# Kernel optimization log

Measured on AMD Instinct MI355X. Metric: run time of the kernel, lower is better.

Reference implementation:

```python
import jax, jax.numpy as jnp
import numpy as np

B, C, M, K, V, D, H, A, L, HF = 2, 128, 4, 4, 64, 1024, 16, 64, 4, 2048
E = M + K
EPS = 1e-5
THETA = 10000.0


def _rmsnorm(x, w):
    return x * jax.lax.rsqrt(jnp.mean(x * x, -1, keepdims=True) + EPS) * w


def _l2norm(x):
    n = jnp.sqrt(jnp.sum(x * x, -1, keepdims=True))
    return x / jnp.maximum(n, EPS)


def _rope(x, cos, sin):
    x1, x2 = jnp.split(x, 2, axis=-1)
    return jnp.concatenate([x1 * cos + x2 * sin, -x1 * sin + x2 * cos], -1)


def _forward(x_input, dec_w1, dec_w2, pos_emb, Wqkv, Wo, Wup, Wdown, attn_norm_w, ffn_norm_w, doc):
    b = x_input.shape[0]
    c = x_input.shape[1] // M
    # decoder_w1 then 'b (c m) (k v) -> b c k (m v)', decoder_w2, pos emb
    x = jnp.einsum('bsd,od->bso', x_input, dec_w1)
    x = x.reshape(b, c, M, K, V).transpose(0, 1, 3, 2, 4).reshape(b, c, K, M * V)
    x = jnp.einsum('bcku,du->bckd', x, dec_w2) + pos_emb
    # decoder_include_original_token: prepend original m tokens per block
    x = jnp.concatenate([x_input.reshape(b, c, M, D), x], axis=2).reshape(b, c * E, D)
    s = c * E
    # mask_mod (decoder_global_original_attn): (causal & kv%e<k & same_doc) | same_block
    idx = jnp.arange(s)
    blk = idx // E
    docs = doc[:, blk]  # [b, s]
    doc_m = docs[:, :, None] == docs[:, None, :]
    causal = blk[:, None] >= blk[None, :]
    kv_ok = (idx % E) < K
    same = blk[:, None] == blk[None, :]
    mask = (causal[None] & kv_ok[None, None, :] & doc_m) | same[None]  # [b, s, s]
    # rotary tables (applied post head-split, dim A)
    inv_freq = (1.0 / THETA) ** (jnp.arange(0, A, 2) / A)
    freqs = jnp.arange(s)[:, None] * inv_freq[None, :]
    cos, sin = jnp.cos(freqs), jnp.sin(freqs)  # [s, A/2]
    scale = 1.0 / jnp.sqrt(jnp.float32(A))
    neg = jnp.float32(-1e30)

    def heads(t):
        return t.reshape(b, s, H, A).transpose(0, 2, 1, 3)

    for li in range(L):
        xn = _rmsnorm(x, attn_norm_w[li])
        qkv = jnp.einsum('bsd,od->bso', xn, Wqkv[li])
        q, k, v = jnp.split(qkv, 3, axis=-1)
        q, k, v = heads(q), heads(k), heads(v)
        q, k = _l2norm(q), _l2norm(k)  # qk_norm
        q, k = _rope(q, cos, sin), _rope(k, cos, sin)
        scores = jnp.einsum('bhqa,bhka->bhqk', q, k) * scale
        scores = jnp.where(mask[:, None], scores, neg)
        probs = jax.nn.softmax(scores, axis=-1)
        attn = jnp.einsum('bhqk,bhka->bhqa', probs, v)
        attn = attn.transpose(0, 2, 1, 3).reshape(b, s, D)
        x1_in = jnp.einsum('bsd,od->bso', attn, Wo[li]) + x
        xf = _rmsnorm(x1_in, ffn_norm_w[li])
        up = jnp.einsum('bsd,od->bso', xf, Wup[li])
        u1, u2 = jnp.split(up, 2, axis=-1)
        x = jnp.einsum('bsh,dh->bsd', jax.nn.silu(u1) * u2, Wdown[li]) + x1_in
    # 'b (c e) d -> (b c) e d' then drop original tokens
    return x.reshape(b * c, E, D)[:, M:]


def setup_inputs() -> dict:
    key = jax.random.key(0)
    ks = jax.random.split(key, 10)
    sc = 0.02
    return {
        'x_input': jax.random.normal(ks[0], (B, C * M, D), jnp.float32),
        'doc': jnp.sort(jax.random.randint(ks[1], (B, C), 0, 4), axis=-1),
        'dec_w1': jax.random.normal(ks[2], (K * V, D), jnp.float32) * sc,
        'dec_w2': jax.random.normal(ks[3], (D, M * V), jnp.float32) * sc,
        'pos_emb': jax.random.normal(ks[4], (1, 1, K, D), jnp.float32) * sc,
        'Wqkv': jax.random.normal(ks[5], (L, 3 * D, D), jnp.float32) * sc,
        'Wo': jax.random.normal(ks[6], (L, D, D), jnp.float32) * sc,
        'Wup': jax.random.normal(ks[7], (L, 2 * HF, D), jnp.float32) * sc,
        'Wdown': jax.random.normal(ks[8], (L, D, HF), jnp.float32) * sc,
        'attn_norm_w': jnp.ones((L, D), jnp.float32),
        'ffn_norm_w': jnp.ones((L, D), jnp.float32),
    }


def reference(x_input, doc, dec_w1, dec_w2, pos_emb, Wqkv, Wo, Wup, Wdown, attn_norm_w, ffn_norm_w):
    return _forward(x_input, dec_w1, dec_w2, pos_emb, Wqkv, Wo, Wup, Wdown, attn_norm_w, ffn_norm_w, doc)
```

## Files before the change

### kernel.cpp

```cpp
#include <hip/hip_runtime.h>
#include <hip/hip_bf16.h>

typedef __bf16 bf16;
typedef __bf16 bf16x8 __attribute__((ext_vector_type(8)));
typedef __bf16 bf16x4 __attribute__((ext_vector_type(4)));
typedef float  f32x4  __attribute__((ext_vector_type(4)));

#define MFMA16(a, b, c) __builtin_amdgcn_mfma_f32_16x16x32_bf16(a, b, c, 0, 0, 0)

template <int EPI, int AF32, int BF32, int TM, int TN>
__global__ __launch_bounds__(256) void gemm_bt(
    const void* __restrict__ Av, const void* __restrict__ Bv,
    const float* __restrict__ Res, void* __restrict__ Out,
    int Ntot, int Ktot, int lda)
{
    constexpr int PA = TM / 64, PB = TN / 64;
    constexpr int WN = (TN == 128) ? ((TM == 128) ? 2 : 4) : 2;
    constexpr int WM = 4 / WN;
    constexpr int I = TM / (WM * 16), J = TN / (WN * 16);
    __shared__ __align__(16) bf16 As[2][TM][40];
    __shared__ __align__(16) bf16 Bs[2][TN][40];
    const int tid  = threadIdx.x;
    const int wave = tid >> 6, lane = tid & 63;
    const int quad = lane >> 4, l16 = lane & 15;
    const int wm = wave / WN, wn = wave % WN;
    const int rowW = wm * (TM / WM), colW = wn * (TN / WN);
    const int rowBase = blockIdx.y * TM, colBase = blockIdx.x * TN;

    f32x4 acc[I][J];
    const f32x4 z4 = {0.f, 0.f, 0.f, 0.f};
#pragma unroll
    for (int i = 0; i < I; i++)
#pragma unroll
        for (int j = 0; j < J; j++) acc[i][j] = z4;

    float4 rAf[PA][2]; bf16x8 rAb[PA];
    float4 rBf[PB][2]; bf16x8 rBb[PB];

    auto loadTile = [&](int kt) {
#pragma unroll
        for (int p = 0; p < PA; p++) {
            int ch = p * 256 + tid, r = ch >> 2, c8 = (ch & 3) << 3;
            if (AF32) {
                const float* s = (const float*)Av + (size_t)(rowBase + r) * lda + kt + c8;
                rAf[p][0] = *(const float4*)s; rAf[p][1] = *(const float4*)(s + 4);
            } else {
                rAb[p] = *(const bf16x8*)((const bf16*)Av + (size_t)(rowBase + r) * lda + kt + c8);
            }
        }
#pragma unroll
        for (int p = 0; p < PB; p++) {
            int ch = p * 256 + tid, r = ch >> 2, c8 = (ch & 3) << 3;
            if (BF32) {
                const float* s = (const float*)Bv + (size_t)(colBase + r) * Ktot + kt + c8;
                rBf[p][0] = *(const float4*)s; rBf[p][1] = *(const float4*)(s + 4);
            } else {
                rBb[p] = *(const bf16x8*)((const bf16*)Bv + (size_t)(colBase + r) * Ktot + kt + c8);
            }
        }
    };
    auto storeTile = [&](int buf) {
#pragma unroll
        for (int p = 0; p < PA; p++) {
            int ch = p * 256 + tid, r = ch >> 2, c8 = (ch & 3) << 3;
            bf16x8 t;
            if (AF32) {
                t[0]=(bf16)rAf[p][0].x; t[1]=(bf16)rAf[p][0].y; t[2]=(bf16)rAf[p][0].z; t[3]=(bf16)rAf[p][0].w;
                t[4]=(bf16)rAf[p][1].x; t[5]=(bf16)rAf[p][1].y; t[6]=(bf16)rAf[p][1].z; t[7]=(bf16)rAf[p][1].w;
            } else t = rAb[p];
            *(bf16x8*)&As[buf][r][c8] = t;
        }
#pragma unroll
        for (int p = 0; p < PB; p++) {
            int ch = p * 256 + tid, r = ch >> 2, c8 = (ch & 3) << 3;
            bf16x8 t;
            if (BF32) {
                t[0]=(bf16)rBf[p][0].x; t[1]=(bf16)rBf[p][0].y; t[2]=(bf16)rBf[p][0].z; t[3]=(bf16)rBf[p][0].w;
                t[4]=(bf16)rBf[p][1].x; t[5]=(bf16)rBf[p][1].y; t[6]=(bf16)rBf[p][1].z; t[7]=(bf16)rBf[p][1].w;
            } else t = rBb[p];
            *(bf16x8*)&Bs[buf][r][c8] = t;
        }
    };

    loadTile(0);
    storeTile(0);
    __syncthreads();
    const int nk = Ktot >> 5;
    for (int k = 0; k < nk; k++) {
        const bool more = (k + 1) < nk;
        if (more) loadTile((k + 1) << 5);
        const int buf = k & 1;
        bf16x8 af[I], bfr[J];
#pragma unroll
        for (int i = 0; i < I; i++)
            af[i] = *(const bf16x8*)&As[buf][rowW + i * 16 + l16][quad * 8];
#pragma unroll
        for (int j = 0; j < J; j++)
            bfr[j] = *(const bf16x8*)&Bs[buf][colW + j * 16 + l16][quad * 8];
#pragma unroll
        for (int i = 0; i < I; i++)
#pragma unroll
            for (int j = 0; j < J; j++)
                acc[i][j] = MFMA16(af[i], bfr[j], acc[i][j]);
        if (more) { storeTile(buf ^ 1); __syncthreads(); }
    }

#pragma unroll
    for (int i = 0; i < I; i++) {
        int row0 = rowBase + rowW + i * 16 + quad * 4;
#pragma unroll
        for (int j = 0; j < J; j++) {
            int col = colBase + colW + j * 16 + l16;
#pragma unroll
            for (int r = 0; r < 4; r++) {
                size_t off = (size_t)(row0 + r) * Ntot + col;
                float v = acc[i][j][r];
                if (EPI == 0)      ((bf16*)Out)[off]  = (bf16)v;
                else if (EPI == 1) ((float*)Out)[off] = v + Res[off];
                else               ((float*)Out)[off] = v;
            }
        }
    }
}

__global__ __launch_bounds__(256) void gemm_up_swiglu(
    const bf16* __restrict__ A, const float* __restrict__ B,
    bf16* __restrict__ Out)
{
    __shared__ __align__(16) bf16 As[2][128][40];
    __shared__ __align__(16) bf16 Bs[2][128][40];
    const int tid  = threadIdx.x;
    const int wave = tid >> 6, lane = tid & 63;
    const int quad = lane >> 4, l16 = lane & 15;
    const int wm = wave >> 1, wn = wave & 1;
    const int rowBase = blockIdx.y * 128, cb = blockIdx.x;

    f32x4 acc[4][4];
    const f32x4 z4 = {0.f, 0.f, 0.f, 0.f};
#pragma unroll
    for (int i = 0; i < 4; i++)
#pragma unroll
        for (int j = 0; j < 4; j++) acc[i][j] = z4;

    bf16x8 rA[2]; float4 rB[2][2];
    auto loadTile = [&](int kt) {
#pragma unroll
        for (int p = 0; p < 2; p++) {
            int ch = p * 256 + tid, r = ch >> 2, c8 = (ch & 3) << 3;
            rA[p] = *(const bf16x8*)(A + (size_t)(rowBase + r) * 1024 + kt + c8);
            int brow = (r >> 6) * 2048 + cb * 64 + (r & 63);
            const float* s = B + (size_t)brow * 1024 + kt + c8;
            rB[p][0] = *(const float4*)s; rB[p][1] = *(const float4*)(s + 4);
        }
    };
    auto storeTile = [&](int buf) {
#pragma unroll
        for (int p = 0; p < 2; p++) {
            int ch = p * 256 + tid, r = ch >> 2, c8 = (ch & 3) << 3;
            *(bf16x8*)&As[buf][r][c8] = rA[p];
            bf16x8 t;
            t[0]=(bf16)rB[p][0].x; t[1]=(bf16)rB[p][0].y; t[2]=(bf16)rB[p][0].z; t[3]=(bf16)rB[p][0].w;
            t[4]=(bf16)rB[p][1].x; t[5]=(bf16)rB[p][1].y; t[6]=(bf16)rB[p][1].z; t[7]=(bf16)rB[p][1].w;
            *(bf16x8*)&Bs[buf][r][c8] = t;
        }
    };

    loadTile(0);
    storeTile(0);
    __syncthreads();
    for (int k = 0; k < 32; k++) {
        const bool more = k < 31;
        if (more) loadTile((k + 1) << 5);
        const int buf = k & 1;
        bf16x8 af[4], bfr[4];
#pragma unroll
        for (int i = 0; i < 4; i++)
            af[i] = *(const bf16x8*)&As[buf][wm * 64 + i * 16 + l16][quad * 8];
#pragma unroll
        for (int j = 0; j < 4; j++) {
            int brow = (j < 2) ? (wn * 32 + j * 16) : (64 + wn * 32 + (j - 2) * 16);
            bfr[j] = *(const bf16x8*)&Bs[buf][brow + l16][quad * 8];
        }
#pragma unroll
        for (int i = 0; i < 4; i++)
#pragma unroll
            for (int j = 0; j < 4; j++)
                acc[i][j] = MFMA16(af[i], bfr[j], acc[i][j]);
        if (more) { storeTile(buf ^ 1); __syncthreads(); }
    }

#pragma unroll
    for (int i = 0; i < 4; i++) {
        int row0 = rowBase + wm * 64 + i * 16 + quad * 4;
#pragma unroll
        for (int jj = 0; jj < 2; jj++) {
            int col = cb * 64 + wn * 32 + jj * 16 + l16;
#pragma unroll
            for (int r = 0; r < 4; r++) {
                float u1 = acc[i][jj][r], u2 = acc[i][jj + 2][r];
                float g = u1 / (1.f + __expf(-u1));
                Out[(size_t)(row0 + r) * 2048 + col] = (bf16)(g * u2);
            }
        }
    }
}

__global__ __launch_bounds__(256) void rmsnorm_k(
    const float* __restrict__ X, const float* __restrict__ W,
    bf16* __restrict__ Out)
{
    const int row = blockIdx.x, tid = threadIdx.x;
    const float4 xv = *(const float4*)(X + (size_t)row * 1024 + tid * 4);
    float ss = xv.x * xv.x + xv.y * xv.y + xv.z * xv.z + xv.w * xv.w;
#pragma unroll
    for (int m = 1; m < 64; m <<= 1) ss += __shfl_xor(ss, m);
    __shared__ float red[4];
    if ((tid & 63) == 0) red[tid >> 6] = ss;
    __syncthreads();
    float tot = red[0] + red[1] + red[2] + red[3];
    float sc = rsqrtf(tot * (1.0f / 1024.0f) + 1e-5f);
    const float4 wv = *(const float4*)(W + tid * 4);
    bf16x4 o;
    o[0] = (bf16)(xv.x * sc * wv.x);
    o[1] = (bf16)(xv.y * sc * wv.y);
    o[2] = (bf16)(xv.z * sc * wv.z);
    o[3] = (bf16)(xv.w * sc * wv.w);
    *(bf16x4*)(Out + (size_t)row * 1024 + tid * 4) = o;
}

__global__ __launch_bounds__(256) void ropetab_k(float* __restrict__ tab)
{
    int i = blockIdx.x * 256 + threadIdx.x;
    int s = i >> 5, j = i & 31;
    float f = (float)s * __expf(-(float)j * 0.2878231366242557f);
    tab[i * 2]     = cosf(f);
    tab[i * 2 + 1] = sinf(f);
}

__global__ __launch_bounds__(256) void qkprep_k(
    bf16* __restrict__ qkv, const float* __restrict__ tab)
{
    int wid  = blockIdx.x * 4 + (threadIdx.x >> 6);
    int lane = threadIdx.x & 63;
    int s = wid & 1023, h = (wid >> 10) & 15, b = (wid >> 14) & 1, op = wid >> 15;
    bf16* addr = qkv + ((size_t)(b * 1024 + s)) * 3072 + op * 1024 + h * 64 + lane;
    float v = (float)*addr;
    float ss = v * v;
#pragma unroll
    for (int m = 1; m < 64; m <<= 1) ss += __shfl_xor(ss, m);
    v /= fmaxf(sqrtf(ss), 1e-5f);
    float2 cssn = ((const float2*)tab)[(s << 5) + (lane & 31)];
    float partner = __shfl_xor(v, 32);
    float o = (lane < 32) ? (v * cssn.x + partner * cssn.y)
                          : (v * cssn.x - partner * cssn.y);
    *addr = (bf16)o;
}

__global__ __launch_bounds__(256) void vtrans_k(
    const bf16* __restrict__ qkv, bf16* __restrict__ Vt)
{
    __shared__ __align__(16) bf16 Ls[64][72];
    const int st = blockIdx.x, h = blockIdx.y, b = blockIdx.z;
    const int tid = threadIdx.x;
#pragma unroll
    for (int p = 0; p < 2; p++) {
        int s = p * 32 + (tid >> 3), a0 = (tid & 7) << 3;
        *(bf16x8*)&Ls[s][a0] = *(const bf16x8*)(
            qkv + ((size_t)(b * 1024 + st * 64 + s)) * 3072 + 2048 + h * 64 + a0);
    }
    __syncthreads();
#pragma unroll
    for (int p = 0; p < 2; p++) {
        int a = p * 32 + (tid >> 3), s0 = (tid & 7) << 3;
        bf16x8 v;
#pragma unroll
        for (int j = 0; j < 8; j++) v[j] = Ls[s0 + j][a];
        *(bf16x8*)(Vt + (((size_t)((b * 16 + h) * 64 + a)) << 10) + st * 64 + s0) = v;
    }
}

__global__ __launch_bounds__(256) void attn_k(
    const bf16* __restrict__ qkv, const bf16* __restrict__ Vt,
    const int* __restrict__ doc, bf16* __restrict__ attnb)
{
    const int p = blockIdx.x, h = blockIdx.y, b = blockIdx.z;
    const int tid = threadIdx.x, w = tid >> 6, lane = tid & 63;
    const int quad = lane >> 4, l16 = lane & 15;
    const float NEG = -30000.0f;
    __shared__ __align__(16) bf16 PsT[4][64][20];
    __shared__ int docL[128];
    if (tid < 128) docL[tid] = doc[b * 128 + tid];
    __syncthreads();

    const int g = (w == 0) ? p : (w == 1) ? 31 - p : (w == 2) ? 32 + p : 63 - p;
    const bf16* qp = qkv + ((size_t)(b * 1024 + g * 16 + l16)) * 3072 + h * 64 + quad * 8;
    const bf16x8 qf0 = *(const bf16x8*)qp;
    const bf16x8 qf1 = *(const bf16x8*)(qp + 32);
    const bf16* Kbase = qkv + ((size_t)(b * 1024)) * 3072 + 1024 + h * 64;
    const bf16* Vbase = Vt + (((size_t)((b * 16 + h) * 64)) << 10);

    const f32x4 z4 = {0.f, 0.f, 0.f, 0.f};
    f32x4 O[4] = {z4, z4, z4, z4};
    float mrun[4], lrun[4];
#pragma unroll
    for (int r = 0; r < 4; r++) { mrun[r] = NEG; lrun[r] = 0.f; }

    bf16x8 kc[8], kn[8];
    auto loadK = [&](int kt, bf16x8* dst) {
        const bf16* kp = Kbase + (size_t)(kt * 64 + l16) * 3072 + quad * 8;
#pragma unroll
        for (int kg = 0; kg < 4; kg++) {
            dst[kg * 2]     = *(const bf16x8*)(kp + (size_t)kg * 16 * 3072);
            dst[kg * 2 + 1] = *(const bf16x8*)(kp + (size_t)kg * 16 * 3072 + 32);
        }
    };

    const int tiles = (g + 4) >> 2;
    loadK(0, kc);
    for (int kt = 0; kt < tiles; kt++) {
        const int k0 = kt * 64;
        f32x4 sf[4];
#pragma unroll
        for (int kg = 0; kg < 4; kg++) {
            sf[kg] = z4;
            sf[kg] = MFMA16(qf0, kc[kg * 2],     sf[kg]);
            sf[kg] = MFMA16(qf1, kc[kg * 2 + 1], sf[kg]);
        }
        bf16x8 vr[4][2];
#pragma unroll
        for (int t = 0; t < 4; t++)
#pragma unroll
            for (int c = 0; c < 2; c++)
                vr[t][c] = *(const bf16x8*)(
                    Vbase + ((size_t)(t * 16 + l16) << 10) + k0 + c * 32 + quad * 8);
        if (kt + 1 < tiles) loadK(kt + 1, kn);

        float alpha[4], pv[4][4];
#pragma unroll
        for (int r = 0; r < 4; r++) {
            int qg = g * 16 + quad * 4 + r;
            int bq = qg >> 3, dq = docL[bq];
            float sv[4];
#pragma unroll
            for (int kg = 0; kg < 4; kg++) {
                int kgi = k0 + kg * 16 + l16;
                int bk = kgi >> 3;
                bool ok = (bq == bk) || ((bq >= bk) && ((kgi & 7) < 4) && (dq == docL[bk]));
                sv[kg] = ok ? sf[kg][r] * 0.125f : NEG;
            }
            float mr = fmaxf(fmaxf(sv[0], sv[1]), fmaxf(sv[2], sv[3]));
#pragma unroll
            for (int m = 1; m < 16; m <<= 1) mr = fmaxf(mr, __shfl_xor(mr, m));
            float mn = fmaxf(mrun[r], mr);
            alpha[r] = __expf(mrun[r] - mn);
            float ls = 0.f;
#pragma unroll
            for (int kg = 0; kg < 4; kg++) {
                float pp = __expf(sv[kg] - mn);
                pv[kg][r] = pp;
                ls += pp;
            }
#pragma unroll
            for (int m = 1; m < 16; m <<= 1) ls += __shfl_xor(ls, m);
            lrun[r] = lrun[r] * alpha[r] + ls;
            mrun[r] = mn;
        }
#pragma unroll
        for (int kg = 0; kg < 4; kg++) {
            bf16x4 t4;
#pragma unroll
            for (int r = 0; r < 4; r++) t4[r] = (bf16)pv[kg][r];
            *(bf16x4*)&PsT[w][kg * 16 + l16][quad * 4] = t4;
        }
        bf16x8 pa0, pa1;
#pragma unroll
        for (int j = 0; j < 8; j++) {
            pa0[j] = PsT[w][quad * 8 + j][l16];
            pa1[j] = PsT[w][32 + quad * 8 + j][l16];
        }
#pragma unroll
        for (int t = 0; t < 4; t++) {
#pragma unroll
            for (int r = 0; r < 4; r++) O[t][r] *= alpha[r];
            O[t] = MFMA16(pa0, vr[t][0], O[t]);
            O[t] = MFMA16(pa1, vr[t][1], O[t]);
        }
        if (kt + 1 < tiles) {
#pragma unroll
            for (int i = 0; i < 8; i++) kc[i] = kn[i];
        }
    }

#pragma unroll
    for (int t = 0; t < 4; t++)
#pragma unroll
        for (int r = 0; r < 4; r++) {
            int qg = g * 16 + quad * 4 + r;
            float v = O[t][r] / fmaxf(lrun[r], 1e-20f);
            attnb[((size_t)(b * 1024) + qg) * 1024 + h * 64 + t * 16 + l16] = (bf16)v;
        }
}

__global__ __launch_bounds__(256) void permute_k(
    const bf16* __restrict__ t1, bf16* __restrict__ t1p)
{
    int idx = blockIdx.x * 256 + threadIdx.x;
    int u = idx & 255, m = u >> 6, v = u & 63;
    int orow = idx >> 8;
    int k = orow & 3, bc = orow >> 2;
    int b = bc >> 7, c = bc & 127;
    t1p[idx] = t1[((size_t)(b * 512 + c * 4 + m)) * 256 + k * 64 + v];
}

__global__ __launch_bounds__(256) void buildx_k(
    const float* __restrict__ x_input, const float* __restrict__ t2,
    const float* __restrict__ pos_emb, float* __restrict__ xres)
{
    int idx = blockIdx.x * 256 + threadIdx.x;
    int d = idx & 1023, row = idx >> 10;
    int b = row >> 10, rr = row & 1023;
    int c = rr >> 3, e = rr & 7;
    float v;
    if (e < 4)
        v = x_input[((size_t)(b * 512 + c * 4 + e)) * 1024 + d];
    else
        v = t2[((size_t)(b * 512 + c * 4 + (e - 4))) * 1024 + d] +
            pos_emb[(e - 4) * 1024 + d];
    xres[idx] = v;
}

__global__ __launch_bounds__(256) void finalout_k(
    const float* __restrict__ xres, float* __restrict__ out)
{
    int idx = blockIdx.x * 256 + threadIdx.x;
    int d = idx & 1023, t = idx >> 10;
    int kk = t & 3, bc = t >> 2;
    int b = bc >> 7, c = bc & 127;
    out[idx] = xres[((size_t)(b * 1024 + c * 8 + 4 + kk)) * 1024 + d];
}

extern "C" void kernel_launch(void* const* d_in, const int* in_sizes, int n_in,
                              void* d_out, int out_size, void* d_ws, size_t ws_size,
                              hipStream_t stream)
{
    const float* x_input = (const float*)d_in[0];
    const int*   doc     = (const int*)d_in[1];
    const float* dec_w1  = (const float*)d_in[2];
    const float* dec_w2  = (const float*)d_in[3];
    const float* pos_emb = (const float*)d_in[4];
    const float* Wqkv    = (const float*)d_in[5];
    const float* Wo      = (const float*)d_in[6];
    const float* Wup     = (const float*)d_in[7];
    const float* Wdown   = (const float*)d_in[8];
    const float* anw     = (const float*)d_in[9];
    const float* fnw     = (const float*)d_in[10];
    float* out = (float*)d_out;

    char* w = (char*)d_ws;
    float* xres  = (float*)(w);
    bf16*  attnb = (bf16*)(w + (8u << 20));
    bf16*  t1    = (bf16*)(w + (8u << 20));
    bf16*  t1p   = (bf16*)(w + (8u << 20) + (512u << 10));
    bf16*  Vt    = (bf16*)(w + (12u << 20));
    bf16*  xn2   = (bf16*)(w + (12u << 20));
    bf16*  qkv   = (bf16*)(w + (16u << 20));
    float* t2    = (float*)(w + (16u << 20));
    float* x1res = (float*)(w + (16u << 20));
    bf16*  hg    = (bf16*)(w + (24u << 20));
    bf16*  xn1   = (bf16*)(w + (28u << 20));
    float* rtab  = out;

    ropetab_k<<<128, 256, 0, stream>>>(rtab);
    gemm_bt<0, 1, 1, 64, 64><<<dim3(4, 16), 256, 0, stream>>>(
        x_input, dec_w1, nullptr, t1, 256, 1024, 1024);
    permute_k<<<1024, 256, 0, stream>>>(t1, t1p);
    gemm_bt<2, 0, 1, 64, 64><<<dim3(16, 16), 256, 0, stream>>>(
        t1p, dec_w2, nullptr, t2, 1024, 256, 256);
    buildx_k<<<8192, 256, 0, stream>>>(x_input, t2, pos_emb, xres);

    for (int li = 0; li < 4; ++li) {
        rmsnorm_k<<<2048, 256, 0, stream>>>(xres, anw + li * 1024, xn1);
        gemm_bt<0, 0, 1, 128, 128><<<dim3(24, 16), 256, 0, stream>>>(
            xn1, Wqkv + (size_t)li * 3072 * 1024, nullptr, qkv, 3072, 1024, 1024);
        qkprep_k<<<16384, 256, 0, stream>>>(qkv, rtab);
        vtrans_k<<<dim3(16, 16, 2), 256, 0, stream>>>(qkv, Vt);
        attn_k<<<dim3(16, 16, 2), 256, 0, stream>>>(qkv, Vt, doc, attnb);
        gemm_bt<1, 0, 1, 64, 64><<<dim3(16, 32), 256, 0, stream>>>(
            attnb, Wo + (size_t)li * 1024 * 1024, xres, x1res, 1024, 1024, 1024);
        rmsnorm_k<<<2048, 256, 0, stream>>>(x1res, fnw + li * 1024, xn2);
        gemm_up_swiglu<<<dim3(32, 16), 256, 0, stream>>>(
            xn2, Wup + (size_t)li * 4096 * 1024, hg);
        gemm_bt<1, 0, 1, 64, 64><<<dim3(16, 32), 256, 0, stream>>>(
            hg, Wdown + (size_t)li * 1024 * 2048, x1res, xres, 1024, 2048, 2048);
    }

    finalout_k<<<4096, 256, 0, stream>>>(xres, out);
}
```

Baseline: 1.064 ms.

## Drop online-softmax max tracking using bounded L2-normalized scores

Since q and k are L2-normalized, scaled scores lie in [-0.125, 0.125], so the attention kernel now skips the running max, rescale factors and per-tile cross-lane reductions. It exponentiates the masked scores directly and reduces the row sum once at the end. The 1/sqrt(A) scale is folded into the q normalization/rope prep kernel. Per-row block/doc indices are hoisted out of the tile loop. This relies on the qk-norm bound holding and changes bf16 rounding slightly, because q is pre-scaled before the cast.

```diff
diff --git a/kernel.cpp b/kernel.cpp
--- a/kernel.cpp
+++ b/kernel.cpp
@@ -253,6 +253,7 @@
     float partner = __shfl_xor(v, 32);
     float o = (lane < 32) ? (v * cssn.x + partner * cssn.y)
                           : (v * cssn.x - partner * cssn.y);
+    if (op == 0) o *= 0.125f;
     *addr = (bf16)o;
 }
 
@@ -286,7 +287,6 @@
     const int p = blockIdx.x, h = blockIdx.y, b = blockIdx.z;
     const int tid = threadIdx.x, w = tid >> 6, lane = tid & 63;
     const int quad = lane >> 4, l16 = lane & 15;
-    const float NEG = -30000.0f;
     __shared__ __align__(16) bf16 PsT[4][64][20];
     __shared__ int docL[128];
     if (tid < 128) docL[tid] = doc[b * 128 + tid];
@@ -301,9 +301,14 @@
 
     const f32x4 z4 = {0.f, 0.f, 0.f, 0.f};
     f32x4 O[4] = {z4, z4, z4, z4};
-    float mrun[4], lrun[4];
-#pragma unroll
-    for (int r = 0; r < 4; r++) { mrun[r] = NEG; lrun[r] = 0.f; }
+    float lp[4] = {0.f, 0.f, 0.f, 0.f};
+
+    int bq[4], dq[4];
+#pragma unroll
+    for (int r = 0; r < 4; r++) {
+        bq[r] = (g * 16 + quad * 4 + r) >> 3;
+        dq[r] = docL[bq[r]];
+    }
 
     bf16x8 kc[8], kn[8];
     auto loadK = [&](int kt, bf16x8* dst) {
@@ -335,41 +340,26 @@
                     Vbase + ((size_t)(t * 16 + l16) << 10) + k0 + c * 32 + quad * 8);
         if (kt + 1 < tiles) loadK(kt + 1, kn);
 
-        float alpha[4], pv[4][4];
-#pragma unroll
-        for (int r = 0; r < 4; r++) {
-            int qg = g * 16 + quad * 4 + r;
-            int bq = qg >> 3, dq = docL[bq];
-            float sv[4];
-#pragma unroll
-            for (int kg = 0; kg < 4; kg++) {
-                int kgi = k0 + kg * 16 + l16;
-                int bk = kgi >> 3;
-                bool ok = (bq == bk) || ((bq >= bk) && ((kgi & 7) < 4) && (dq == docL[bk]));
-                sv[kg] = ok ? sf[kg][r] * 0.125f : NEG;
+        float pvv[4][4];
+#pragma unroll
+        for (int kg = 0; kg < 4; kg++) {
+            int kgi = k0 + kg * 16 + l16;
+            int bk  = kgi >> 3;
+            int dkv = docL[bk];
+            bool kbit = (kgi & 7) < 4;
+#pragma unroll
+            for (int r = 0; r < 4; r++) {
+                bool ok = (bq[r] == bk) || ((bq[r] >= bk) && kbit && (dq[r] == dkv));
+                float pp = ok ? __expf(sf[kg][r]) : 0.f;
+                pvv[kg][r] = pp;
+                lp[r] += pp;
             }
-            float mr = fmaxf(fmaxf(sv[0], sv[1]), fmaxf(sv[2], sv[3]));
-#pragma unroll
-            for (int m = 1; m < 16; m <<= 1) mr = fmaxf(mr, __shfl_xor(mr, m));
-            float mn = fmaxf(mrun[r], mr);
-            alpha[r] = __expf(mrun[r] - mn);
-            float ls = 0.f;
-#pragma unroll
-            for (int kg = 0; kg < 4; kg++) {
-                float pp = __expf(sv[kg] - mn);
-                pv[kg][r] = pp;
-                ls += pp;
-            }
-#pragma unroll
-            for (int m = 1; m < 16; m <<= 1) ls += __shfl_xor(ls, m);
-            lrun[r] = lrun[r] * alpha[r] + ls;
-            mrun[r] = mn;
         }
 #pragma unroll
         for (int kg = 0; kg < 4; kg++) {
             bf16x4 t4;
 #pragma unroll
-            for (int r = 0; r < 4; r++) t4[r] = (bf16)pv[kg][r];
+            for (int r = 0; r < 4; r++) t4[r] = (bf16)pvv[kg][r];
             *(bf16x4*)&PsT[w][kg * 16 + l16][quad * 4] = t4;
         }
         bf16x8 pa0, pa1;
@@ -380,8 +370,6 @@
         }
 #pragma unroll
         for (int t = 0; t < 4; t++) {
-#pragma unroll
-            for (int r = 0; r < 4; r++) O[t][r] *= alpha[r];
             O[t] = MFMA16(pa0, vr[t][0], O[t]);
             O[t] = MFMA16(pa1, vr[t][1], O[t]);
         }
@@ -392,11 +380,17 @@
     }
 
 #pragma unroll
+    for (int r = 0; r < 4; r++) {
+#pragma unroll
+        for (int m = 1; m < 16; m <<= 1) lp[r] += __shfl_xor(lp[r], m);
+    }
+
+#pragma unroll
     for (int t = 0; t < 4; t++)
 #pragma unroll
         for (int r = 0; r < 4; r++) {
             int qg = g * 16 + quad * 4 + r;
-            float v = O[t][r] / fmaxf(lrun[r], 1e-20f);
+            float v = O[t][r] / fmaxf(lp[r], 1e-20f);
             attnb[((size_t)(b * 1024) + qg) * 1024 + h * 64 + t * 16 + l16] = (bf16)v;
         }
 }
```

Result: faster. 1.000 ms (-6.0%).
